# Optimization experiments

Hardware: AMD Instinct MI355X
Metric: run time of the kernel (lower is better)

Reference implementation:

```python
import jax, jax.numpy as jnp
import numpy as np

B, C, CO, H, W = 64, 64, 64, 56, 56
E, K = 8, 2


def _conv3x3(x, k, b):
    # x: [B,C,H,W], k: [CO,C,3,3], b: [CO]
    y = jax.lax.conv_general_dilated(
        x, k, window_strides=(1, 1), padding='SAME',
        dimension_numbers=('NCHW', 'OIHW', 'NCHW'))
    return y + b[None, :, None, None]


def setup_inputs() -> dict:
    key = jax.random.key(0)
    k1, k2, k3, k4, k5 = jax.random.split(key, 5)
    x = jax.random.normal(k1, (B, C, H, W), dtype=jnp.float32)
    weights = jax.random.uniform(k2, (B, K), dtype=jnp.float32)
    indices = jax.random.randint(k3, (B, K), 0, E, dtype=jnp.int32)
    W_exp = jax.random.normal(k4, (E, CO, C, 3, 3), dtype=jnp.float32) * 0.05
    b_exp = jax.random.normal(k5, (E, CO), dtype=jnp.float32) * 0.01
    return {'x': x, 'weights': weights, 'indices': indices,
            'W_exp': W_exp, 'b_exp': b_exp}


def reference(x, weights, indices, W_exp, b_exp):
    # Dense-equivalent MoE dispatch: run every expert on the full batch,
    # then gather the top-k expert outputs per sample and combine.
    # Same math as the masked gather / index_add_ loop in the torch module.
    # acts: [E, B, CO, H, W]
    acts = jax.vmap(lambda k, b: jax.nn.relu(_conv3x3(x, k, b)))(W_exp, b_exp)
    acts_b = jnp.transpose(acts, (1, 0, 2, 3, 4))  # [B, E, CO, H, W]
    idx = indices[:, :, None, None, None].astype(jnp.int32)
    sel = jnp.take_along_axis(acts_b, idx, axis=1)  # [B, K, CO, H, W]
    out = jnp.sum(sel * weights[:, :, None, None, None], axis=1)  # [B, CO, H, W]
    return out
```

## Files before the change

kernel.cpp:

```cpp
#include <hip/hip_runtime.h>


#define BB 64
#define CC 64
#define COO 64
#define HH 56
#define WW 56

typedef __bf16 bf16x8 __attribute__((ext_vector_type(8)));
typedef float  f32x4  __attribute__((ext_vector_type(4)));

__global__ __launch_bounds__(256) void prep_kernel(
    const float* __restrict__ x, const float* __restrict__ Wexp,
    __bf16* __restrict__ xT, __bf16* __restrict__ Wpack)
{
    const int bx  = blockIdx.x;
    const int tid = threadIdx.x;

    if (bx < 960) {
        __shared__ float tile[CC][WW + 1];
        const int b   = bx / 15;
        const int grp = bx - b * 15;
        #pragma unroll 1
        for (int rr = 0; rr < 4; ++rr) {
            const int hp = grp * 4 + rr;
            if (hp >= 58) break;
            __bf16* dst = xT + ((size_t)b * 58 + hp) * 66 * CC;
            const bool interior = (hp >= 1 && hp <= HH);
            if (!interior) {
                bf16x8 z = {};
                for (int j = tid; j < 66 * CC / 8; j += 256)
                    *(bf16x8*)(dst + j * 8) = z;
                continue;
            }
            const int h = hp - 1;
            const float* xb = x + (size_t)b * CC * HH * WW + (size_t)h * WW;
            for (int i = tid; i < CC * 14; i += 256) {
                const int c = i / 14, wq = i - c * 14;
                const float4 f = *(const float4*)(xb + (size_t)c * HH * WW + wq * 4);
                tile[c][wq * 4 + 0] = f.x; tile[c][wq * 4 + 1] = f.y;
                tile[c][wq * 4 + 2] = f.z; tile[c][wq * 4 + 3] = f.w;
            }
            __syncthreads();
            for (int j = tid; j < 66 * 8; j += 256) {
                const int wc = j >> 3, cg = j & 7;
                bf16x8 v = {};
                if (wc >= 1 && wc <= WW) {
                    const int w = wc - 1;
                    #pragma unroll
                    for (int u = 0; u < 8; ++u)
                        v[u] = (__bf16)tile[cg * 8 + u][w];
                }
                *(bf16x8*)(dst + wc * CC + cg * 8) = v;
            }
            __syncthreads();
        }
    } else {
        const int wp = bx - 960;
        const int e  = wp / 9, rs = wp - e * 9;
        const int r  = rs / 3, s  = rs - r * 3;
        for (int idx = tid; idx < 4096; idx += 256) {
            const int ks   = idx >> 11;
            const int rem  = idx & 2047;
            const int mt   = rem >> 9;
            const int lane = (rem >> 3) & 63;
            const int j    = idx & 7;
            const int co = mt * 16 + (lane & 15);
            const int c  = ks * 32 + ((lane >> 4) << 3) + j;
            const float v = Wexp[((((size_t)e * COO + co) * CC + c) * 3 + r) * 3 + s];
            Wpack[(size_t)e * 36864 + (size_t)rs * 4096 + idx] = (__bf16)v;
        }
    }
}

__global__ __launch_bounds__(256, 2) void moe_conv_mfma(
    const __bf16* __restrict__ xT, const __bf16* __restrict__ Wpack,
    const float* __restrict__ gate_w, const int* __restrict__ gate_i,
    const float* __restrict__ bexp, float* __restrict__ out)
{
    __shared__ __bf16 ldsA[2 * 12288];

    const int b   = blockIdx.y;
    const int h0  = blockIdx.x * 4;
    const int tid = threadIdx.x;
    const int wid = tid >> 6, lane = tid & 63;
    const int n15 = lane & 15, quad = lane >> 4;
    const int wcol = wid * 16 + n15;

    const int   e0 = gate_i[b * 2 + 0], e1 = gate_i[b * 2 + 1];
    const float g0 = gate_w[b * 2 + 0], g1 = gate_w[b * 2 + 1];

    const __bf16* xb = xT + (size_t)b * 58 * 66 * CC;

    f32x4 acc[2][4][4] = {};

    for (int r = 0; r < 3; ++r) {
        __syncthreads();
        {
            const __bf16* s0 = Wpack + (size_t)e0 * 36864 + r * 12288;
            const __bf16* s1 = Wpack + (size_t)e1 * 36864 + r * 12288;
            #pragma unroll
            for (int i = 0; i < 12; ++i) {
                const int q    = wid * 12 + i;
                const int slot = q >= 24;
                const int rem  = q - slot * 24;
                const __bf16* src = (slot ? s1 : s0) + rem * 512 + lane * 8;
                const uint4 tmp = *(const uint4*)src;
                *(uint4*)&ldsA[q * 512 + lane * 8] = tmp;
            }
        }
        __syncthreads();

        #pragma unroll
        for (int s = 0; s < 3; ++s) {
            #pragma unroll
            for (int ks = 0; ks < 2; ++ks) {
                bf16x8 bf[4];
                #pragma unroll
                for (int t = 0; t < 4; ++t) {
                    const int hr1 = h0 + t + r;
                    const int wc1 = wcol + s;
                    bf[t] = *(const bf16x8*)(
                        xb + (size_t)(hr1 * 66 + wc1) * CC + ks * 32 + quad * 8);
                }
                #pragma unroll
                for (int slot = 0; slot < 2; ++slot) {
                    #pragma unroll
                    for (int mt = 0; mt < 4; ++mt) {
                        const bf16x8 af = *(const bf16x8*)
                            &ldsA[slot * 12288 + (s * 2 + ks) * 2048 + mt * 512 + lane * 8];
                        #pragma unroll
                        for (int t = 0; t < 4; ++t)
                            acc[slot][mt][t] = __builtin_amdgcn_mfma_f32_16x16x32_bf16(
                                af, bf[t], acc[slot][mt][t], 0, 0, 0);
                    }
                }
            }
        }
    }

    if (wcol < WW) {
        #pragma unroll
        for (int t = 0; t < 4; ++t) {
            const int h = h0 + t;
            #pragma unroll
            for (int mt = 0; mt < 4; ++mt) {
                #pragma unroll
                for (int v = 0; v < 4; ++v) {
                    const int co = mt * 16 + quad * 4 + v;
                    float a0 = acc[0][mt][t][v] + bexp[e0 * COO + co];
                    float a1 = acc[1][mt][t][v] + bexp[e1 * COO + co];
                    a0 = fmaxf(a0, 0.f);
                    a1 = fmaxf(a1, 0.f);
                    out[(((size_t)b * COO + co) * HH + h) * WW + wcol] =
                        g0 * a0 + g1 * a1;
                }
            }
        }
    }
}

extern "C" void kernel_launch(void* const* d_in, const int* in_sizes, int n_in,
                              void* d_out, int out_size, void* d_ws, size_t ws_size,
                              hipStream_t stream) {
    const float* x      = (const float*)d_in[0];
    const float* gate_w = (const float*)d_in[1];
    const int*   gate_i = (const int*)  d_in[2];
    const float* Wexp   = (const float*)d_in[3];
    const float* bexp   = (const float*)d_in[4];
    float* out = (float*)d_out;

    __bf16* Wpack = (__bf16*)d_ws;
    __bf16* xT    = (__bf16*)((char*)d_ws + 589824);

    prep_kernel<<<dim3(1032), 256, 0, stream>>>(x, Wexp, xT, Wpack);
    moe_conv_mfma<<<dim3(14, BB), 256, 0, stream>>>(xT, Wpack, gate_w, gate_i,
                                                    bexp, out);
}
```

Measured before the change: 161.7 us.

## Fuse input transpose into conv kernel via swizzled LDS tile, read weights from global

Removes the separate x transpose/pad pass: each conv block now loads its 6 input rows from fp32 global, converts to bf16 and writes them into a zero-padded, XOR-swizzled LDS tile. Weight fragments, which used to be staged in LDS, are now read directly from global (L2-cached) per MFMA. This saves the round trip of the transposed xT buffer through HBM and the per-r weight-staging barriers. In exchange, neighbouring blocks reload halo rows, the scalar bf16 LDS stores are slow, and weight loads now hit global memory inside the inner loop.

```diff
diff --git a/kernel.cpp b/kernel.cpp
--- a/kernel.cpp
+++ b/kernel.cpp
@@ -10,75 +10,32 @@
 typedef __bf16 bf16x8 __attribute__((ext_vector_type(8)));
 typedef float  f32x4  __attribute__((ext_vector_type(4)));
 
-__global__ __launch_bounds__(256) void prep_kernel(
-    const float* __restrict__ x, const float* __restrict__ Wexp,
-    __bf16* __restrict__ xT, __bf16* __restrict__ Wpack)
+__global__ __launch_bounds__(256) void wpack_kernel(
+    const float* __restrict__ Wexp, __bf16* __restrict__ Wpack)
 {
-    const int bx  = blockIdx.x;
+    const int wp  = blockIdx.x;
     const int tid = threadIdx.x;
-
-    if (bx < 960) {
-        __shared__ float tile[CC][WW + 1];
-        const int b   = bx / 15;
-        const int grp = bx - b * 15;
-        #pragma unroll 1
-        for (int rr = 0; rr < 4; ++rr) {
-            const int hp = grp * 4 + rr;
-            if (hp >= 58) break;
-            __bf16* dst = xT + ((size_t)b * 58 + hp) * 66 * CC;
-            const bool interior = (hp >= 1 && hp <= HH);
-            if (!interior) {
-                bf16x8 z = {};
-                for (int j = tid; j < 66 * CC / 8; j += 256)
-                    *(bf16x8*)(dst + j * 8) = z;
-                continue;
-            }
-            const int h = hp - 1;
-            const float* xb = x + (size_t)b * CC * HH * WW + (size_t)h * WW;
-            for (int i = tid; i < CC * 14; i += 256) {
-                const int c = i / 14, wq = i - c * 14;
-                const float4 f = *(const float4*)(xb + (size_t)c * HH * WW + wq * 4);
-                tile[c][wq * 4 + 0] = f.x; tile[c][wq * 4 + 1] = f.y;
-                tile[c][wq * 4 + 2] = f.z; tile[c][wq * 4 + 3] = f.w;
-            }
-            __syncthreads();
-            for (int j = tid; j < 66 * 8; j += 256) {
-                const int wc = j >> 3, cg = j & 7;
-                bf16x8 v = {};
-                if (wc >= 1 && wc <= WW) {
-                    const int w = wc - 1;
-                    #pragma unroll
-                    for (int u = 0; u < 8; ++u)
-                        v[u] = (__bf16)tile[cg * 8 + u][w];
-                }
-                *(bf16x8*)(dst + wc * CC + cg * 8) = v;
-            }
-            __syncthreads();
-        }
-    } else {
-        const int wp = bx - 960;
-        const int e  = wp / 9, rs = wp - e * 9;
-        const int r  = rs / 3, s  = rs - r * 3;
-        for (int idx = tid; idx < 4096; idx += 256) {
-            const int ks   = idx >> 11;
-            const int rem  = idx & 2047;
-            const int mt   = rem >> 9;
-            const int lane = (rem >> 3) & 63;
-            const int j    = idx & 7;
-            const int co = mt * 16 + (lane & 15);
-            const int c  = ks * 32 + ((lane >> 4) << 3) + j;
-            const float v = Wexp[((((size_t)e * COO + co) * CC + c) * 3 + r) * 3 + s];
-            Wpack[(size_t)e * 36864 + (size_t)rs * 4096 + idx] = (__bf16)v;
-        }
+    const int e  = wp / 9, rs = wp - e * 9;
+    const int r  = rs / 3, s  = rs - r * 3;
+    for (int idx = tid; idx < 4096; idx += 256) {
+        const int ks   = idx >> 11;
+        const int rem  = idx & 2047;
+        const int mt   = rem >> 9;
+        const int lane = (rem >> 3) & 63;
+        const int j    = idx & 7;
+        const int co = mt * 16 + (lane & 15);
+        const int c  = ks * 32 + ((lane >> 4) << 3) + j;
+        const float v = Wexp[((((size_t)e * COO + co) * CC + c) * 3 + r) * 3 + s];
+        Wpack[(size_t)e * 36864 + (size_t)rs * 4096 + idx] = (__bf16)v;
     }
 }
 
-__global__ __launch_bounds__(256, 2) void moe_conv_mfma(
-    const __bf16* __restrict__ xT, const __bf16* __restrict__ Wpack,
+__global__ __launch_bounds__(256, 2) void moe_conv_fused(
+    const float* __restrict__ x, const __bf16* __restrict__ Wpack,
     const float* __restrict__ gate_w, const int* __restrict__ gate_i,
     const float* __restrict__ bexp, float* __restrict__ out)
 {
-    __shared__ __bf16 ldsA[2 * 12288];
+    __shared__ __align__(16) __bf16 xt[6 * 66 * CC];
 
     const int b   = blockIdx.y;
     const int h0  = blockIdx.x * 4;
@@ -87,48 +44,67 @@
     const int n15 = lane & 15, quad = lane >> 4;
     const int wcol = wid * 16 + n15;
 
+    {
+        bf16x8 z = {};
+        for (int i = tid; i < 6 * 66 * CC / 8; i += 256)
+            *(bf16x8*)(xt + i * 8) = z;
+    }
+    __syncthreads();
+
+    {
+        const int c  = tid & 63;
+        const int tg = tid >> 6;
+        const float* xb = x + ((size_t)b * CC + c) * (HH * WW);
+        char* xtb = (char*)xt;
+        #pragma unroll
+        for (int lr = 0; lr < 6; ++lr) {
+            const int h = h0 + lr - 1;
+            if (h < 0 || h >= HH) continue;
+            for (int wq = tg; wq < 14; wq += 4) {
+                const float4 f = *(const float4*)(xb + (size_t)h * WW + wq * 4);
+                const float fv[4] = {f.x, f.y, f.z, f.w};
+                #pragma unroll
+                for (int u = 0; u < 4; ++u) {
+                    const int wc = wq * 4 + u + 1;
+                    const int byte = (lr * 66 + wc) * 128 +
+                                     ((c * 2) ^ ((wc & 7) << 4));
+                    *(__bf16*)(xtb + byte) = (__bf16)fv[u];
+                }
+            }
+        }
+    }
+    __syncthreads();
+
     const int   e0 = gate_i[b * 2 + 0], e1 = gate_i[b * 2 + 1];
     const float g0 = gate_w[b * 2 + 0], g1 = gate_w[b * 2 + 1];
-
-    const __bf16* xb = xT + (size_t)b * 58 * 66 * CC;
+    const __bf16* w0 = Wpack + (size_t)e0 * 36864;
+    const __bf16* w1 = Wpack + (size_t)e1 * 36864;
 
     f32x4 acc[2][4][4] = {};
 
+    #pragma unroll
     for (int r = 0; r < 3; ++r) {
-        __syncthreads();
-        {
-            const __bf16* s0 = Wpack + (size_t)e0 * 36864 + r * 12288;
-            const __bf16* s1 = Wpack + (size_t)e1 * 36864 + r * 12288;
-            #pragma unroll
-            for (int i = 0; i < 12; ++i) {
-                const int q    = wid * 12 + i;
-                const int slot = q >= 24;
-                const int rem  = q - slot * 24;
-                const __bf16* src = (slot ? s1 : s0) + rem * 512 + lane * 8;
-                const uint4 tmp = *(const uint4*)src;
-                *(uint4*)&ldsA[q * 512 + lane * 8] = tmp;
-            }
-        }
-        __syncthreads();
-
         #pragma unroll
         for (int s = 0; s < 3; ++s) {
+            const int wc1 = wcol + s;
+            const int sw  = (wc1 & 7) << 4;
             #pragma unroll
             for (int ks = 0; ks < 2; ++ks) {
                 bf16x8 bf[4];
                 #pragma unroll
                 for (int t = 0; t < 4; ++t) {
-                    const int hr1 = h0 + t + r;
-                    const int wc1 = wcol + s;
-                    bf[t] = *(const bf16x8*)(
-                        xb + (size_t)(hr1 * 66 + wc1) * CC + ks * 32 + quad * 8);
+                    const int lr = t + r;
+                    const int byte = (lr * 66 + wc1) * 128 +
+                                     ((ks * 64 + quad * 16) ^ sw);
+                    bf[t] = *(const bf16x8*)((const char*)xt + byte);
                 }
+                const size_t rsks = (size_t)(r * 3 + s) * 4096 + ks * 2048;
                 #pragma unroll
                 for (int slot = 0; slot < 2; ++slot) {
+                    const __bf16* wp = (slot ? w1 : w0) + rsks + lane * 8;
                     #pragma unroll
                     for (int mt = 0; mt < 4; ++mt) {
-                        const bf16x8 af = *(const bf16x8*)
-                            &ldsA[slot * 12288 + (s * 2 + ks) * 2048 + mt * 512 + lane * 8];
+                        const bf16x8 af = *(const bf16x8*)(wp + mt * 512);
                         #pragma unroll
                         for (int t = 0; t < 4; ++t)
                             acc[slot][mt][t] = __builtin_amdgcn_mfma_f32_16x16x32_bf16(
@@ -171,9 +147,8 @@
     float* out = (float*)d_out;
 
     __bf16* Wpack = (__bf16*)d_ws;
-    __bf16* xT    = (__bf16*)((char*)d_ws + 589824);
 
-    prep_kernel<<<dim3(1032), 256, 0, stream>>>(x, Wexp, xT, Wpack);
-    moe_conv_mfma<<<dim3(14, BB), 256, 0, stream>>>(xT, Wpack, gate_w, gate_i,
-                                                    bexp, out);
+    wpack_kernel<<<dim3(72), 256, 0, stream>>>(Wexp, Wpack);
+    moe_conv_fused<<<dim3(14, BB), 256, 0, stream>>>(x, Wpack, gate_w, gate_i,
+                                                     bexp, out);
 }
```

New measurement: 184.4 us. 14.0% more time.

## Split output channels across blocks, double-buffer weights via direct LDS loads, relayout input

Applied to the files above, without the earlier changes.

Changes the padded input layout from channel-innermost to channel-group-major rows, so each lane's B-fragment loads become contiguous across the column dimension. The conv kernel now splits the 64 output channels into two halves per block. That halves the accumulators and shrinks LDS to a double-buffered 8 KB, which allows occupancy 4. Weight staging uses global_load_lds, prefetching the next filter tap while computing the current one, and a swizzled 1D grid groups blocks for locality. The cost is that each input tile is read twice, once per channel half.

```diff
diff --git a/kernel.cpp b/kernel.cpp
--- a/kernel.cpp
+++ b/kernel.cpp
@@ -25,11 +25,11 @@
         for (int rr = 0; rr < 4; ++rr) {
             const int hp = grp * 4 + rr;
             if (hp >= 58) break;
-            __bf16* dst = xT + ((size_t)b * 58 + hp) * 66 * CC;
+            __bf16* dst = xT + ((size_t)b * 58 + hp) * 4224;
             const bool interior = (hp >= 1 && hp <= HH);
             if (!interior) {
                 bf16x8 z = {};
-                for (int j = tid; j < 66 * CC / 8; j += 256)
+                for (int j = tid; j < 4224 / 8; j += 256)
                     *(bf16x8*)(dst + j * 8) = z;
                 continue;
             }
@@ -43,7 +43,8 @@
             }
             __syncthreads();
             for (int j = tid; j < 66 * 8; j += 256) {
-                const int wc = j >> 3, cg = j & 7;
+                const int cg = j / 66;
+                const int wc = j - cg * 66;
                 bf16x8 v = {};
                 if (wc >= 1 && wc <= WW) {
                     const int w = wc - 1;
@@ -51,7 +52,7 @@
                     for (int u = 0; u < 8; ++u)
                         v[u] = (__bf16)tile[cg * 8 + u][w];
                 }
-                *(bf16x8*)(dst + wc * CC + cg * 8) = v;
+                *(bf16x8*)(dst + j * 8) = v;
             }
             __syncthreads();
         }
@@ -73,15 +74,20 @@
     }
 }
 
-__global__ __launch_bounds__(256, 2) void moe_conv_mfma(
+__global__ __launch_bounds__(256, 4) void moe_conv_mfma(
     const __bf16* __restrict__ xT, const __bf16* __restrict__ Wpack,
     const float* __restrict__ gate_w, const int* __restrict__ gate_i,
     const float* __restrict__ bexp, float* __restrict__ out)
 {
-    __shared__ __bf16 ldsA[2 * 12288];
+    __shared__ __align__(16) __bf16 ldsA[2 * 4096];
 
-    const int b   = blockIdx.y;
-    const int h0  = blockIdx.x * 4;
+    const int bid = blockIdx.x;
+    const int swz = (bid & 7) * 224 + (bid >> 3);
+    const int b   = swz / 28;
+    const int rem = swz - b * 28;
+    const int h0  = (rem >> 1) * 4;
+    const int mh  = rem & 1;
+
     const int tid = threadIdx.x;
     const int wid = tid >> 6, lane = tid & 63;
     const int n15 = lane & 15, quad = lane >> 4;
@@ -89,54 +95,54 @@
 
     const int   e0 = gate_i[b * 2 + 0], e1 = gate_i[b * 2 + 1];
     const float g0 = gate_w[b * 2 + 0], g1 = gate_w[b * 2 + 1];
+    const __bf16* w0 = Wpack + (size_t)e0 * 36864;
+    const __bf16* w1 = Wpack + (size_t)e1 * 36864;
 
-    const __bf16* xb = xT + (size_t)b * 58 * 66 * CC;
+    auto stage = [&](int rsn, int bufn) {
+        #pragma unroll
+        for (int i = 0; i < 2; ++i) {
+            const __bf16* src = (wid >= 2 ? w1 : w0) + (size_t)rsn * 4096
+                              + (wid & 1) * 2048 + (mh * 2 + i) * 512 + lane * 8;
+            __bf16* dstp = &ldsA[bufn * 4096 + (wid * 2 + i) * 512 + lane * 8];
+            __builtin_amdgcn_global_load_lds(
+                (const __attribute__((address_space(1))) unsigned int*)src,
+                (__attribute__((address_space(3))) unsigned int*)dstp, 16, 0, 0);
+        }
+    };
 
-    f32x4 acc[2][4][4] = {};
+    const __bf16* pq = xT + (size_t)b * 244992 + quad * 528 + wcol * 8;
 
-    for (int r = 0; r < 3; ++r) {
+    f32x4 acc[2][2][4] = {};
+
+    stage(0, 0);
+    int r = 0, s = 0;
+    #pragma unroll 1
+    for (int rs = 0; rs < 9; ++rs) {
+        const int buf = rs & 1;
         __syncthreads();
-        {
-            const __bf16* s0 = Wpack + (size_t)e0 * 36864 + r * 12288;
-            const __bf16* s1 = Wpack + (size_t)e1 * 36864 + r * 12288;
+        if (rs < 8) stage(rs + 1, buf ^ 1);
+
+        const __bf16* pb = pq + (size_t)(h0 + r) * 4224 + s * 8;
+        #pragma unroll
+        for (int ks = 0; ks < 2; ++ks) {
+            bf16x8 bf[4];
             #pragma unroll
-            for (int i = 0; i < 12; ++i) {
-                const int q    = wid * 12 + i;
-                const int slot = q >= 24;
-                const int rem  = q - slot * 24;
-                const __bf16* src = (slot ? s1 : s0) + rem * 512 + lane * 8;
-                const uint4 tmp = *(const uint4*)src;
-                *(uint4*)&ldsA[q * 512 + lane * 8] = tmp;
-            }
-        }
-        __syncthreads();
-
-        #pragma unroll
-        for (int s = 0; s < 3; ++s) {
+            for (int t = 0; t < 4; ++t)
+                bf[t] = *(const bf16x8*)(pb + t * 4224 + ks * 2112);
             #pragma unroll
-            for (int ks = 0; ks < 2; ++ks) {
-                bf16x8 bf[4];
+            for (int slot = 0; slot < 2; ++slot) {
                 #pragma unroll
-                for (int t = 0; t < 4; ++t) {
-                    const int hr1 = h0 + t + r;
-                    const int wc1 = wcol + s;
-                    bf[t] = *(const bf16x8*)(
-                        xb + (size_t)(hr1 * 66 + wc1) * CC + ks * 32 + quad * 8);
-                }
-                #pragma unroll
-                for (int slot = 0; slot < 2; ++slot) {
+                for (int mtl = 0; mtl < 2; ++mtl) {
+                    const bf16x8 af = *(const bf16x8*)
+                        &ldsA[buf * 4096 + slot * 2048 + ks * 1024 + mtl * 512 + lane * 8];
                     #pragma unroll
-                    for (int mt = 0; mt < 4; ++mt) {
-                        const bf16x8 af = *(const bf16x8*)
-                            &ldsA[slot * 12288 + (s * 2 + ks) * 2048 + mt * 512 + lane * 8];
-                        #pragma unroll
-                        for (int t = 0; t < 4; ++t)
-                            acc[slot][mt][t] = __builtin_amdgcn_mfma_f32_16x16x32_bf16(
-                                af, bf[t], acc[slot][mt][t], 0, 0, 0);
-                    }
+                    for (int t = 0; t < 4; ++t)
+                        acc[slot][mtl][t] = __builtin_amdgcn_mfma_f32_16x16x32_bf16(
+                            af, bf[t], acc[slot][mtl][t], 0, 0, 0);
                 }
             }
         }
+        if (++s == 3) { s = 0; ++r; }
     }
 
     if (wcol < WW) {
@@ -144,12 +150,12 @@
         for (int t = 0; t < 4; ++t) {
             const int h = h0 + t;
             #pragma unroll
-            for (int mt = 0; mt < 4; ++mt) {
+            for (int mtl = 0; mtl < 2; ++mtl) {
                 #pragma unroll
                 for (int v = 0; v < 4; ++v) {
-                    const int co = mt * 16 + quad * 4 + v;
-                    float a0 = acc[0][mt][t][v] + bexp[e0 * COO + co];
-                    float a1 = acc[1][mt][t][v] + bexp[e1 * COO + co];
+                    const int co = (mh * 2 + mtl) * 16 + quad * 4 + v;
+                    float a0 = acc[0][mtl][t][v] + bexp[e0 * COO + co];
+                    float a1 = acc[1][mtl][t][v] + bexp[e1 * COO + co];
                     a0 = fmaxf(a0, 0.f);
                     a1 = fmaxf(a1, 0.f);
                     out[(((size_t)b * COO + co) * HH + h) * WW + wcol] =
@@ -174,6 +180,6 @@
     __bf16* xT    = (__bf16*)((char*)d_ws + 589824);
 
     prep_kernel<<<dim3(1032), 256, 0, stream>>>(x, Wexp, xT, Wpack);
-    moe_conv_mfma<<<dim3(14, BB), 256, 0, stream>>>(xT, Wpack, gate_w, gate_i,
-                                                    bexp, out);
+    moe_conv_mfma<<<dim3(1792), 256, 0, stream>>>(xT, Wpack, gate_w, gate_i,
+                                                  bexp, out);
 }
```

Result: faster. 147.6 us (-8.8%).
